# Optimization experiments

Hardware: AMD Instinct MI355X
Metric: run time of the kernel (lower is better)

## Reference

```python
import jax, jax.numpy as jnp
import numpy as np
import math

SIZE = 11
PAD = 5
C1 = 0.01 ** 2
C2 = 0.03 ** 2


def gaussian_window():
    # Matches torch __init__: 1D gaussian (sigma=1.5), normalized, outer product,
    # expanded to depthwise weight of shape (3, 1, 11, 11)
    x = np.arange(SIZE, dtype=np.float32)
    g = np.exp(-((x - SIZE // 2) ** 2) / (2.0 * 1.5 ** 2)).astype(np.float32)
    g = g / g.sum()
    w2d = np.outer(g, g).astype(np.float32)  # (11, 11)
    return jnp.asarray(np.broadcast_to(w2d, (3, 1, SIZE, SIZE)).copy())


def depthwise_conv(x, win):
    return jax.lax.conv_general_dilated(
        x, win,
        window_strides=(1, 1),
        padding=[(PAD, PAD), (PAD, PAD)],
        dimension_numbers=('NCHW', 'OIHW', 'NCHW'),
        feature_group_count=3,
    )


def setup_inputs() -> dict:
    key = jax.random.key(0)
    k1, k2 = jax.random.split(key)
    img1 = jax.random.uniform(k1, (16, 3, 512, 512), dtype=jnp.float32)
    img2 = jax.random.uniform(k2, (16, 3, 512, 512), dtype=jnp.float32)
    return {"img1": img1, "img2": img2, "win": gaussian_window()}


def reference(img1, img2, win):
    mu1 = depthwise_conv(img1, win)
    mu2 = depthwise_conv(img2, win)
    mu1_sq = mu1 * mu1
    mu2_sq = mu2 * mu2
    mu1_mu2 = mu1 * mu2
    sig1_sq = depthwise_conv(img1 * img1, win) - mu1_sq
    sig2_sq = depthwise_conv(img2 * img2, win) - mu2_sq
    sig12 = depthwise_conv(img1 * img2, win) - mu1_mu2
    v = ((2.0 * mu1_mu2 + C1) * (2.0 * sig12 + C2)) / (
        (mu1_sq + mu2_sq + C1) * (sig1_sq + sig2_sq + C2))
    return 1.0 - jnp.mean(v)
```

## Files before the change

### kernel.cpp

```cpp
#include <hip/hip_runtime.h>


#define IMG 512
#define NPIX (16LL * 3 * 512 * 512)
#define NBLK (8 * 16 * 48)
#define NPART (NBLK * 4)
#define HP 56

typedef short v8s __attribute__((ext_vector_type(8)));
typedef float v4f __attribute__((ext_vector_type(4)));
typedef __bf16 bf2 __attribute__((ext_vector_type(2)));
typedef float f2  __attribute__((ext_vector_type(2)));

__device__ __forceinline__ int cvtpk(float lo, float hi) {
    f2 f; f.x = lo; f.y = hi;
    bf2 r = __builtin_convertvector(f, bf2);
    return __builtin_bit_cast(int, r);
}
__device__ __forceinline__ unsigned f2bf(float f) {
    unsigned u = __float_as_uint(f);
    return (u + 0x7FFFu + ((u >> 16) & 1u)) >> 16;
}

template <bool EDGE>
__device__ __forceinline__ void hpass(
    const float* __restrict__ p1, const float* __restrict__ p2,
    int tx0, int ty0, int lm, int quad, int ct, v8s band,
    short (*hw)[16][HP])
{
    const v4f zacc = {0.f, 0.f, 0.f, 0.f};
    #pragma unroll
    for (int rt = 0; rt < 3; ++rt) {
        const int grow = ty0 - 8 + rt * 16 + lm;
        const int gcol = tx0 - 8 + ct * 16 + quad * 8;
        float4 a0, a1, b0, b1;
        if (!EDGE) {
            const float* r1 = p1 + (size_t)grow * IMG + gcol;
            const float* r2 = p2 + (size_t)grow * IMG + gcol;
            a0 = *(const float4*)r1;       a1 = *(const float4*)(r1 + 4);
            b0 = *(const float4*)r2;       b1 = *(const float4*)(r2 + 4);
        } else {
            float4 z4; z4.x = z4.y = z4.z = z4.w = 0.f;
            a0 = a1 = b0 = b1 = z4;
            if ((unsigned)grow < IMG) {
                const float* r1 = p1 + (size_t)grow * IMG;
                const float* r2 = p2 + (size_t)grow * IMG;
                if ((unsigned)gcol < IMG) {
                    a0 = *(const float4*)(r1 + gcol);
                    b0 = *(const float4*)(r2 + gcol);
                }
                if ((unsigned)(gcol + 4) < IMG) {
                    a1 = *(const float4*)(r1 + gcol + 4);
                    b1 = *(const float4*)(r2 + gcol + 4);
                }
            }
        }
        v8s A[4];
        int4 w;
        w.x = cvtpk(a0.x, a0.y); w.y = cvtpk(a0.z, a0.w);
        w.z = cvtpk(a1.x, a1.y); w.w = cvtpk(a1.z, a1.w);
        A[0] = __builtin_bit_cast(v8s, w);
        w.x = cvtpk(b0.x, b0.y); w.y = cvtpk(b0.z, b0.w);
        w.z = cvtpk(b1.x, b1.y); w.w = cvtpk(b1.z, b1.w);
        A[1] = __builtin_bit_cast(v8s, w);
        w.x = cvtpk(fmaf(a0.x, a0.x, b0.x * b0.x), fmaf(a0.y, a0.y, b0.y * b0.y));
        w.y = cvtpk(fmaf(a0.z, a0.z, b0.z * b0.z), fmaf(a0.w, a0.w, b0.w * b0.w));
        w.z = cvtpk(fmaf(a1.x, a1.x, b1.x * b1.x), fmaf(a1.y, a1.y, b1.y * b1.y));
        w.w = cvtpk(fmaf(a1.z, a1.z, b1.z * b1.z), fmaf(a1.w, a1.w, b1.w * b1.w));
        A[2] = __builtin_bit_cast(v8s, w);
        w.x = cvtpk(a0.x * b0.x, a0.y * b0.y);
        w.y = cvtpk(a0.z * b0.z, a0.w * b0.w);
        w.z = cvtpk(a1.x * b1.x, a1.y * b1.y);
        w.w = cvtpk(a1.z * b1.z, a1.w * b1.w);
        A[3] = __builtin_bit_cast(v8s, w);

        #pragma unroll
        for (int p = 0; p < 4; ++p) {
            const v4f acc = __builtin_amdgcn_mfma_f32_16x16x32_bf16(A[p], band, zacc, 0, 0, 0);
            int2 w2;
            w2.x = cvtpk(acc[0], acc[1]);
            w2.y = cvtpk(acc[2], acc[3]);
            *(int2*)&hw[p][lm][rt * 16 + quad * 4] = w2;
        }
    }
}

__global__ __launch_bounds__(256, 5) void ssim_kernel(
    const float* __restrict__ img1,
    const float* __restrict__ img2,
    const float* __restrict__ win,
    float* __restrict__ partial)
{
    __shared__ __align__(16) short hbuf[4][4][16][HP];

    const int tid  = threadIdx.x;
    const int lane = tid & 63;
    const int wave = tid >> 6;
    const int lm   = lane & 15;
    const int quad = lane >> 4;

    const int bx = blockIdx.x, by = blockIdx.y, z = blockIdx.z;
    const int tx0 = bx * 64, ty0 = by * 32;

    float gl = 0.f;
    if (lane < 11) gl = win[55 + lane] * rsqrtf(win[60]);
    v8s band;
    #pragma unroll
    for (int j = 0; j < 8; ++j) {
        const int t  = quad * 8 + j - lm - 3;
        const int tc = ((unsigned)t > 10u) ? 11 : t;
        band[j] = (short)f2bf(__shfl(gl, tc));
    }

    const size_t zoff = (size_t)z * IMG * IMG;
    const float* p1 = img1 + zoff;
    const float* p2 = img2 + zoff;

    const bool interior = (bx > 0) & (bx < 7) & (by > 0) & (by < 15);
    if (interior) hpass<false>(p1, p2, tx0, ty0, lm, quad, wave, band, hbuf[wave]);
    else          hpass<true >(p1, p2, tx0, ty0, lm, quad, wave, band, hbuf[wave]);

    const v4f zacc = {0.f, 0.f, 0.f, 0.f};
    const float C1c = 1e-4f;
    const float C2c = 9e-4f;
    float vsum = 0.f;
    #pragma unroll
    for (int t2 = 0; t2 < 2; ++t2) {
        const int r0v = t2 * 16;
        v4f acc[4];
        #pragma unroll
        for (int p = 0; p < 4; ++p) {
            const v8s hf = *(const v8s*)&hbuf[wave][p][lm][r0v + quad * 8];
            acc[p] = __builtin_amdgcn_mfma_f32_16x16x32_bf16(band, hf, zacc, 0, 0, 0);
        }
        #pragma unroll
        for (int r = 0; r < 4; ++r) {
            const float m1 = acc[0][r], m2 = acc[1][r];
            const float es = acc[2][r], ex = acc[3][r];
            const float m1s = m1 * m1, m2s = m2 * m2, m12 = m1 * m2;
            const float sig = es - m1s - m2s;
            const float s12 = ex - m12;
            const float num = (2.f * m12 + C1c) * (2.f * s12 + C2c);
            const float den = (m1s + m2s + C1c) * (sig + C2c);
            vsum += num * __builtin_amdgcn_rcpf(den);
        }
    }

    #pragma unroll
    for (int off = 32; off > 0; off >>= 1)
        vsum += __shfl_down(vsum, off, 64);
    if (lane == 0) {
        const int bidx = (z * (int)gridDim.y + by) * (int)gridDim.x + bx;
        partial[bidx * 4 + wave] = vsum;
    }
}

__global__ __launch_bounds__(512) void finalize_kernel(
    const float* __restrict__ partial, float* __restrict__ out)
{
    __shared__ float red[8];
    const float4* p4 = (const float4*)partial;
    float s = 0.f;
    for (int i = threadIdx.x; i < NPART / 4; i += 512) {
        float4 t = p4[i];
        s += (t.x + t.y) + (t.z + t.w);
    }
    #pragma unroll
    for (int off = 32; off > 0; off >>= 1)
        s += __shfl_down(s, off, 64);
    if ((threadIdx.x & 63) == 0) red[threadIdx.x >> 6] = s;
    __syncthreads();
    if (threadIdx.x == 0) {
        float t = 0.f;
        #pragma unroll
        for (int i = 0; i < 8; ++i) t += red[i];
        out[0] = 1.0f - t / (float)NPIX;
    }
}

extern "C" void kernel_launch(void* const* d_in, const int* in_sizes, int n_in,
                              void* d_out, int out_size, void* d_ws, size_t ws_size,
                              hipStream_t stream) {
    const float* img1 = (const float*)d_in[0];
    const float* img2 = (const float*)d_in[1];
    const float* win  = (const float*)d_in[2];
    float* partialb = (float*)d_ws;

    dim3 grid(IMG / 64, IMG / 32, 48);
    ssim_kernel<<<grid, dim3(256), 0, stream>>>(img1, img2, win, partialb);
    finalize_kernel<<<1, dim3(512), 0, stream>>>(partialb, (float*)d_out);
}
```

Measured before the change: 147.4 us.

## Process two column tiles per wave with loads hoisted ahead and packed f32 math

Each block now covers 128 columns instead of 64, so each wave handles two 16-column tiles. Global loads for both tiles are issued up front, before any compute, so the second tile's memory latency overlaps the first tile's work. Elementwise work is rewritten with 2-wide float vectors to encourage packed FP32 instructions. The grid halves and the occupancy hint drops from 5 to 4, which raises register pressure and gives fewer blocks to hide latency.

```diff
diff --git a/kernel.cpp b/kernel.cpp
--- a/kernel.cpp
+++ b/kernel.cpp
@@ -3,7 +3,9 @@
 
 #define IMG 512
 #define NPIX (16LL * 3 * 512 * 512)
-#define NBLK (8 * 16 * 48)
+#define GX 4
+#define GY 16
+#define NBLK (GX * GY * 48)
 #define NPART (NBLK * 4)
 #define HP 56
 
@@ -12,80 +14,120 @@
 typedef __bf16 bf2 __attribute__((ext_vector_type(2)));
 typedef float f2  __attribute__((ext_vector_type(2)));
 
-__device__ __forceinline__ int cvtpk(float lo, float hi) {
-    f2 f; f.x = lo; f.y = hi;
-    bf2 r = __builtin_convertvector(f, bf2);
+static __device__ __forceinline__ int cvtpk2(f2 v) {
+    bf2 r = __builtin_convertvector(v, bf2);
     return __builtin_bit_cast(int, r);
 }
-__device__ __forceinline__ unsigned f2bf(float f) {
+static __device__ __forceinline__ unsigned f2bf(float f) {
     unsigned u = __float_as_uint(f);
     return (u + 0x7FFFu + ((u >> 16) & 1u)) >> 16;
 }
 
+struct Tile { float4 a[3][2]; float4 b[3][2]; };
+
 template <bool EDGE>
-__device__ __forceinline__ void hpass(
+static __device__ __forceinline__ void load_tile(
     const float* __restrict__ p1, const float* __restrict__ p2,
-    int tx0, int ty0, int lm, int quad, int ct, v8s band,
-    short (*hw)[16][HP])
-{
-    const v4f zacc = {0.f, 0.f, 0.f, 0.f};
+    int tx0, int ty0, int ct, int lm, int quad, Tile& t)
+{
     #pragma unroll
     for (int rt = 0; rt < 3; ++rt) {
         const int grow = ty0 - 8 + rt * 16 + lm;
         const int gcol = tx0 - 8 + ct * 16 + quad * 8;
-        float4 a0, a1, b0, b1;
         if (!EDGE) {
             const float* r1 = p1 + (size_t)grow * IMG + gcol;
             const float* r2 = p2 + (size_t)grow * IMG + gcol;
-            a0 = *(const float4*)r1;       a1 = *(const float4*)(r1 + 4);
-            b0 = *(const float4*)r2;       b1 = *(const float4*)(r2 + 4);
+            t.a[rt][0] = *(const float4*)r1;  t.a[rt][1] = *(const float4*)(r1 + 4);
+            t.b[rt][0] = *(const float4*)r2;  t.b[rt][1] = *(const float4*)(r2 + 4);
         } else {
             float4 z4; z4.x = z4.y = z4.z = z4.w = 0.f;
-            a0 = a1 = b0 = b1 = z4;
+            t.a[rt][0] = t.a[rt][1] = t.b[rt][0] = t.b[rt][1] = z4;
             if ((unsigned)grow < IMG) {
                 const float* r1 = p1 + (size_t)grow * IMG;
                 const float* r2 = p2 + (size_t)grow * IMG;
                 if ((unsigned)gcol < IMG) {
-                    a0 = *(const float4*)(r1 + gcol);
-                    b0 = *(const float4*)(r2 + gcol);
+                    t.a[rt][0] = *(const float4*)(r1 + gcol);
+                    t.b[rt][0] = *(const float4*)(r2 + gcol);
                 }
                 if ((unsigned)(gcol + 4) < IMG) {
-                    a1 = *(const float4*)(r1 + gcol + 4);
-                    b1 = *(const float4*)(r2 + gcol + 4);
+                    t.a[rt][1] = *(const float4*)(r1 + gcol + 4);
+                    t.b[rt][1] = *(const float4*)(r2 + gcol + 4);
                 }
             }
         }
-        v8s A[4];
-        int4 w;
-        w.x = cvtpk(a0.x, a0.y); w.y = cvtpk(a0.z, a0.w);
-        w.z = cvtpk(a1.x, a1.y); w.w = cvtpk(a1.z, a1.w);
+    }
+}
+
+static __device__ __forceinline__ void compute_tile(
+    const Tile& t, v8s band, short (*hw)[16][HP],
+    int lm, int quad, f2& vsum)
+{
+    const v4f zacc = {0.f, 0.f, 0.f, 0.f};
+    #pragma unroll
+    for (int rt = 0; rt < 3; ++rt) {
+        const float4 a0 = t.a[rt][0], a1 = t.a[rt][1];
+        const float4 b0 = t.b[rt][0], b1 = t.b[rt][1];
+        f2 a0l; a0l.x = a0.x; a0l.y = a0.y;   f2 a0h; a0h.x = a0.z; a0h.y = a0.w;
+        f2 a1l; a1l.x = a1.x; a1l.y = a1.y;   f2 a1h; a1h.x = a1.z; a1h.y = a1.w;
+        f2 b0l; b0l.x = b0.x; b0l.y = b0.y;   f2 b0h; b0h.x = b0.z; b0h.y = b0.w;
+        f2 b1l; b1l.x = b1.x; b1l.y = b1.y;   f2 b1h; b1h.x = b1.z; b1h.y = b1.w;
+
+        v8s A[4]; int4 w;
+        w.x = cvtpk2(a0l); w.y = cvtpk2(a0h); w.z = cvtpk2(a1l); w.w = cvtpk2(a1h);
         A[0] = __builtin_bit_cast(v8s, w);
-        w.x = cvtpk(b0.x, b0.y); w.y = cvtpk(b0.z, b0.w);
-        w.z = cvtpk(b1.x, b1.y); w.w = cvtpk(b1.z, b1.w);
+        w.x = cvtpk2(b0l); w.y = cvtpk2(b0h); w.z = cvtpk2(b1l); w.w = cvtpk2(b1h);
         A[1] = __builtin_bit_cast(v8s, w);
-        w.x = cvtpk(fmaf(a0.x, a0.x, b0.x * b0.x), fmaf(a0.y, a0.y, b0.y * b0.y));
-        w.y = cvtpk(fmaf(a0.z, a0.z, b0.z * b0.z), fmaf(a0.w, a0.w, b0.w * b0.w));
-        w.z = cvtpk(fmaf(a1.x, a1.x, b1.x * b1.x), fmaf(a1.y, a1.y, b1.y * b1.y));
-        w.w = cvtpk(fmaf(a1.z, a1.z, b1.z * b1.z), fmaf(a1.w, a1.w, b1.w * b1.w));
+        w.x = cvtpk2(__builtin_elementwise_fma(a0l, a0l, b0l * b0l));
+        w.y = cvtpk2(__builtin_elementwise_fma(a0h, a0h, b0h * b0h));
+        w.z = cvtpk2(__builtin_elementwise_fma(a1l, a1l, b1l * b1l));
+        w.w = cvtpk2(__builtin_elementwise_fma(a1h, a1h, b1h * b1h));
         A[2] = __builtin_bit_cast(v8s, w);
-        w.x = cvtpk(a0.x * b0.x, a0.y * b0.y);
-        w.y = cvtpk(a0.z * b0.z, a0.w * b0.w);
-        w.z = cvtpk(a1.x * b1.x, a1.y * b1.y);
-        w.w = cvtpk(a1.z * b1.z, a1.w * b1.w);
+        w.x = cvtpk2(a0l * b0l); w.y = cvtpk2(a0h * b0h);
+        w.z = cvtpk2(a1l * b1l); w.w = cvtpk2(a1h * b1h);
         A[3] = __builtin_bit_cast(v8s, w);
 
         #pragma unroll
         for (int p = 0; p < 4; ++p) {
             const v4f acc = __builtin_amdgcn_mfma_f32_16x16x32_bf16(A[p], band, zacc, 0, 0, 0);
             int2 w2;
-            w2.x = cvtpk(acc[0], acc[1]);
-            w2.y = cvtpk(acc[2], acc[3]);
+            f2 lo; lo.x = acc[0]; lo.y = acc[1];
+            f2 hi; hi.x = acc[2]; hi.y = acc[3];
+            w2.x = cvtpk2(lo); w2.y = cvtpk2(hi);
             *(int2*)&hw[p][lm][rt * 16 + quad * 4] = w2;
         }
     }
-}
-
-__global__ __launch_bounds__(256, 5) void ssim_kernel(
+
+    const f2 C1v = {1e-4f, 1e-4f};
+    const f2 C2v = {9e-4f, 9e-4f};
+    const f2 two = {2.f, 2.f};
+    #pragma unroll
+    for (int t2 = 0; t2 < 2; ++t2) {
+        const int r0v = t2 * 16;
+        v4f acc[4];
+        #pragma unroll
+        for (int p = 0; p < 4; ++p) {
+            const v8s hf = *(const v8s*)&hw[p][lm][r0v + quad * 8];
+            acc[p] = __builtin_amdgcn_mfma_f32_16x16x32_bf16(band, hf, zacc, 0, 0, 0);
+        }
+        #pragma unroll
+        for (int h = 0; h < 2; ++h) {
+            f2 m1; m1.x = acc[0][2 * h]; m1.y = acc[0][2 * h + 1];
+            f2 m2; m2.x = acc[1][2 * h]; m2.y = acc[1][2 * h + 1];
+            f2 es; es.x = acc[2][2 * h]; es.y = acc[2][2 * h + 1];
+            f2 ex; ex.x = acc[3][2 * h]; ex.y = acc[3][2 * h + 1];
+            const f2 m1s = m1 * m1, m2s = m2 * m2, m12 = m1 * m2;
+            const f2 sig = es - m1s - m2s;
+            const f2 s12 = ex - m12;
+            const f2 num = __builtin_elementwise_fma(two, m12, C1v) *
+                           __builtin_elementwise_fma(two, s12, C2v);
+            const f2 den = (m1s + m2s + C1v) * (sig + C2v);
+            f2 r; r.x = __builtin_amdgcn_rcpf(den.x); r.y = __builtin_amdgcn_rcpf(den.y);
+            vsum = __builtin_elementwise_fma(num, r, vsum);
+        }
+    }
+}
+
+__global__ __launch_bounds__(256, 4) void ssim_kernel(
     const float* __restrict__ img1,
     const float* __restrict__ img2,
     const float* __restrict__ win,
@@ -100,7 +142,7 @@
     const int quad = lane >> 4;
 
     const int bx = blockIdx.x, by = blockIdx.y, z = blockIdx.z;
-    const int tx0 = bx * 64, ty0 = by * 32;
+    const int tx0 = bx * 128, ty0 = by * 32;
 
     float gl = 0.f;
     if (lane < 11) gl = win[55 + lane] * rsqrtf(win[60]);
@@ -116,42 +158,29 @@
     const float* p1 = img1 + zoff;
     const float* p2 = img2 + zoff;
 
-    const bool interior = (bx > 0) & (bx < 7) & (by > 0) & (by < 15);
-    if (interior) hpass<false>(p1, p2, tx0, ty0, lm, quad, wave, band, hbuf[wave]);
-    else          hpass<true >(p1, p2, tx0, ty0, lm, quad, wave, band, hbuf[wave]);
-
-    const v4f zacc = {0.f, 0.f, 0.f, 0.f};
-    const float C1c = 1e-4f;
-    const float C2c = 9e-4f;
-    float vsum = 0.f;
-    #pragma unroll
-    for (int t2 = 0; t2 < 2; ++t2) {
-        const int r0v = t2 * 16;
-        v4f acc[4];
-        #pragma unroll
-        for (int p = 0; p < 4; ++p) {
-            const v8s hf = *(const v8s*)&hbuf[wave][p][lm][r0v + quad * 8];
-            acc[p] = __builtin_amdgcn_mfma_f32_16x16x32_bf16(band, hf, zacc, 0, 0, 0);
-        }
-        #pragma unroll
-        for (int r = 0; r < 4; ++r) {
-            const float m1 = acc[0][r], m2 = acc[1][r];
-            const float es = acc[2][r], ex = acc[3][r];
-            const float m1s = m1 * m1, m2s = m2 * m2, m12 = m1 * m2;
-            const float sig = es - m1s - m2s;
-            const float s12 = ex - m12;
-            const float num = (2.f * m12 + C1c) * (2.f * s12 + C2c);
-            const float den = (m1s + m2s + C1c) * (sig + C2c);
-            vsum += num * __builtin_amdgcn_rcpf(den);
-        }
-    }
-
+    const int ct0 = wave * 2, ct1 = wave * 2 + 1;
+    const bool interior = (bx > 0) & (bx < GX - 1) & (by > 0) & (by < GY - 1);
+
+    Tile t0, t1;
+    if (interior) {
+        load_tile<false>(p1, p2, tx0, ty0, ct0, lm, quad, t0);
+        load_tile<false>(p1, p2, tx0, ty0, ct1, lm, quad, t1);
+    } else {
+        load_tile<true >(p1, p2, tx0, ty0, ct0, lm, quad, t0);
+        load_tile<true >(p1, p2, tx0, ty0, ct1, lm, quad, t1);
+    }
+
+    f2 vsum = {0.f, 0.f};
+    compute_tile(t0, band, hbuf[wave], lm, quad, vsum);
+    compute_tile(t1, band, hbuf[wave], lm, quad, vsum);
+
+    float vs = vsum.x + vsum.y;
     #pragma unroll
     for (int off = 32; off > 0; off >>= 1)
-        vsum += __shfl_down(vsum, off, 64);
+        vs += __shfl_down(vs, off, 64);
     if (lane == 0) {
         const int bidx = (z * (int)gridDim.y + by) * (int)gridDim.x + bx;
-        partial[bidx * 4 + wave] = vsum;
+        partial[bidx * 4 + wave] = vs;
     }
 }
 
@@ -186,7 +215,7 @@
     const float* win  = (const float*)d_in[2];
     float* partialb = (float*)d_ws;
 
-    dim3 grid(IMG / 64, IMG / 32, 48);
+    dim3 grid(GX, GY, 48);
     ssim_kernel<<<grid, dim3(256), 0, stream>>>(img1, img2, win, partialb);
     finalize_kernel<<<1, dim3(512), 0, stream>>>(partialb, (float*)d_out);
 }
```

Result: slower. 153.6 us (+4.2%).
